# Kernel tuning notes

Measured on AMD Instinct MI355X. Metric: run time of the kernel, lower is better.

The kernel has to match this reference:

```python
import jax, jax.numpy as jnp
import numpy as np

N_NODES = 50000
N_EDGES = 800000
N_GRAPHS = 128
D = 128
L = 4
C = 10
GN_EPS = 1e-5


def setup_inputs() -> dict:
    key = jax.random.key(0)
    ks = jax.random.split(key, 12)
    s = 0.05
    x = jax.random.normal(ks[0], (N_NODES, D), dtype=jnp.float32)
    gin_w1 = jax.random.normal(ks[1], (L, D, D), dtype=jnp.float32) * s
    gin_b1 = jax.random.normal(ks[2], (L, D), dtype=jnp.float32) * s
    gin_w2 = jax.random.normal(ks[3], (L, D, D), dtype=jnp.float32) * s
    gin_b2 = jax.random.normal(ks[4], (L, D), dtype=jnp.float32) * s
    gn_weight = jnp.ones((L, D), dtype=jnp.float32)
    gn_bias = jnp.zeros((L, D), dtype=jnp.float32)
    gn_scale = jnp.ones((L, D), dtype=jnp.float32)
    fw1 = jax.random.normal(ks[5], (D, D), dtype=jnp.float32) * s
    fb1 = jnp.zeros((D,), dtype=jnp.float32)
    fw2 = jax.random.normal(ks[6], (D, D), dtype=jnp.float32) * s
    fb2 = jnp.zeros((D,), dtype=jnp.float32)
    fw3 = jax.random.normal(ks[7], (D, C), dtype=jnp.float32) * s
    fb3 = jnp.zeros((C,), dtype=jnp.float32)
    edge_index = jax.random.randint(ks[8], (2, N_EDGES), 0, N_NODES, dtype=jnp.int64)
    batch = jnp.sort(jax.random.randint(ks[9], (N_NODES,), 0, N_GRAPHS, dtype=jnp.int64))
    return dict(x=x, gin_w1=gin_w1, gin_b1=gin_b1, gin_w2=gin_w2, gin_b2=gin_b2,
                gn_weight=gn_weight, gn_bias=gn_bias, gn_scale=gn_scale,
                fw1=fw1, fb1=fb1, fw2=fw2, fb2=fb2, fw3=fw3, fb3=fb3,
                edge_index=edge_index, batch=batch)


def _graph_norm(h, batch, weight, bias, mean_scale, counts):
    # PyG GraphNorm: per-graph mean/var with learnable mean_scale.
    mean = jax.ops.segment_sum(h, batch, num_segments=N_GRAPHS) / counts  # [G, D]
    out = h - mean[batch] * mean_scale
    var = jax.ops.segment_sum(out * out, batch, num_segments=N_GRAPHS) / counts
    return weight * out / jnp.sqrt(var[batch] + GN_EPS) + bias


def reference(x, gin_w1, gin_b1, gin_w2, gin_b2, gn_weight, gn_bias, gn_scale,
              fw1, fb1, fw2, fb2, fw3, fb3, edge_index, batch):
    src, dst = edge_index[0], edge_index[1]
    ones = jnp.ones((N_NODES, 1), dtype=x.dtype)
    counts = jnp.maximum(jax.ops.segment_sum(ones, batch, num_segments=N_GRAPHS), 1.0)  # [G,1]
    h = x
    for l in range(L):
        # GINConv, eps=0: (1+eps)*x + sum_{j->i} x_j, then MLP with act after each Linear
        agg = jax.ops.segment_sum(h[src], dst, num_segments=N_NODES)  # [N, D]
        h = h + agg
        h = jax.nn.relu(h @ gin_w1[l] + gin_b1[l])
        h = jax.nn.relu(h @ gin_w2[l] + gin_b2[l])
        h = _graph_norm(h, batch, gn_weight[l], gn_bias[l], gn_scale[l], counts)
        h = jax.nn.relu(h)
    # sum readout per graph
    g = jax.ops.segment_sum(h, batch, num_segments=N_GRAPHS)  # [G, D]
    # final MLP (dropout is identity in eval)
    g = jax.nn.relu(g @ fw1 + fb1)
    g = jax.nn.relu(g @ fw2 + fb2)
    out = g @ fw3 + fb3
    return jax.nn.log_softmax(out, axis=-1)
```

## Files before the change

kernel.cpp:

```cpp
#include <hip/hip_runtime.h>
#include <cstddef>

#define N_NODES 50000
#define N_EDGES 800000
#define N_GRAPHS 128
#define DIM 128
#define N_LAYERS 4
#define GN_EPS 1e-5f

#define B_CHUNK 256
#define EPB 3125
#define BUCKET_SHIFT 9
#define BUCKET_SIZE 512
#define NB 98

typedef unsigned short ushort_t;
typedef __attribute__((ext_vector_type(8))) short frag8;
typedef __attribute__((ext_vector_type(4))) float f32x4;

__device__ inline float bfbits2f(unsigned hi16) { return __uint_as_float(hi16 << 16); }
__device__ inline ushort_t bf16rne(float v) {
    unsigned u = __float_as_uint(v);
    unsigned r = u + 0x7fff + ((u >> 16) & 1);
    return (ushort_t)(r >> 16);
}
__device__ inline unsigned packbf2(float a, float b) {
    return (unsigned)bf16rne(a) | ((unsigned)bf16rne(b) << 16);
}
__device__ inline void bf16split(float v, ushort_t& h, ushort_t& l) {
    ushort_t hi = bf16rne(v);
    float fh = __uint_as_float(((unsigned)hi) << 16);
    l = bf16rne(v - fh);
    h = hi;
}

__global__ __launch_bounds__(256) void graph_bounds(const int* __restrict__ batch, int* __restrict__ gstart) {
    int i = blockIdx.x * 256 + threadIdx.x;
    if (i >= N_NODES) return;
    int b = batch[i];
    if (i == 0) {
        for (int g = 0; g <= b; ++g) gstart[g] = 0;
    } else {
        int pb = batch[i - 1];
        for (int g = pb + 1; g <= b; ++g) gstart[g] = i;
    }
    if (i == N_NODES - 1) {
        for (int g = b + 1; g <= N_GRAPHS; ++g) gstart[g] = N_NODES;
    }
}

__global__ __launch_bounds__(256) void p1_count(const int* __restrict__ dst, int* __restrict__ cnts) {
    __shared__ int cnt[NB];
    int t = threadIdx.x, blk = blockIdx.x;
    for (int i = t; i < NB; i += 256) cnt[i] = 0;
    __syncthreads();
    int base = blk * EPB;
    for (int i = t; i < EPB; i += 256) atomicAdd(&cnt[dst[base + i] >> BUCKET_SHIFT], 1);
    __syncthreads();
    for (int i = t; i < NB; i += 256) cnts[i * B_CHUNK + blk] = cnt[i];
}

__global__ __launch_bounds__(1024) void scan_local(const int* __restrict__ in, int* __restrict__ out,
                                                   int* __restrict__ bsum, int n) {
    __shared__ int wsum[16];
    int tid = threadIdx.x, lane = tid & 63, w = tid >> 6;
    int gi = blockIdx.x * 1024 + tid;
    int v = (gi < n) ? in[gi] : 0;
    int s = v;
    #pragma unroll
    for (int off = 1; off < 64; off <<= 1) {
        int t = __shfl_up(s, off, 64);
        if (lane >= off) s += t;
    }
    if (lane == 63) wsum[w] = s;
    __syncthreads();
    if (w == 0) {
        int ws = (lane < 16) ? wsum[lane] : 0;
        #pragma unroll
        for (int off = 1; off < 16; off <<= 1) {
            int t = __shfl_up(ws, off, 64);
            if (lane >= off) ws += t;
        }
        if (lane < 16) wsum[lane] = ws;
    }
    __syncthreads();
    int woff = (w > 0) ? wsum[w - 1] : 0;
    if (gi < n) out[gi] = woff + s - v;
    if (tid == 1023) bsum[blockIdx.x] = woff + s;
}

__global__ __launch_bounds__(64) void scan_block(int* __restrict__ bsum, int nb) {
    int lane = threadIdx.x;
    int v = (lane < nb) ? bsum[lane] : 0;
    int s = v;
    #pragma unroll
    for (int off = 1; off < 64; off <<= 1) {
        int t = __shfl_up(s, off, 64);
        if (lane >= off) s += t;
    }
    if (lane < nb) bsum[lane] = s - v;
}

__global__ __launch_bounds__(1024) void scan_add(int* __restrict__ out, const int* __restrict__ bsum, int n, int total) {
    int gi = blockIdx.x * 1024 + threadIdx.x;
    if (gi < n) out[gi] += bsum[blockIdx.x];
    if (blockIdx.x == 0 && threadIdx.x == 0) out[n] = total;
}

__global__ __launch_bounds__(256) void p3_place(const int* __restrict__ src, const int* __restrict__ dst,
                                                const int* __restrict__ off, unsigned* __restrict__ ebuf) {
    __shared__ int cur[NB];
    int t = threadIdx.x, blk = blockIdx.x;
    for (int i = t; i < NB; i += 256) cur[i] = off[i * B_CHUNK + blk];
    __syncthreads();
    int base = blk * EPB;
    for (int i = t; i < EPB; i += 256) {
        int d = dst[base + i];
        int b = d >> BUCKET_SHIFT;
        int pos = atomicAdd(&cur[b], 1);
        ebuf[pos] = (unsigned)src[base + i] | ((unsigned)(d & (BUCKET_SIZE - 1)) << 16);
    }
}

__global__ __launch_bounds__(512) void p4_csr(const unsigned* __restrict__ ebuf, const int* __restrict__ off,
                                              int* __restrict__ eoff, int* __restrict__ csr) {
    __shared__ int cnt[BUCKET_SIZE];
    __shared__ int wsum[8];
    int k = blockIdx.x, t = threadIdx.x;
    int bstart = off[k * B_CHUNK];
    int bend = off[(k + 1) * B_CHUNK];
    cnt[t] = 0;
    __syncthreads();
    for (int i = bstart + t; i < bend; i += 512) atomicAdd(&cnt[ebuf[i] >> 16], 1);
    __syncthreads();
    int lane = t & 63, w = t >> 6;
    int v = cnt[t], s = v;
    #pragma unroll
    for (int o = 1; o < 64; o <<= 1) {
        int tt = __shfl_up(s, o, 64);
        if (lane >= o) s += tt;
    }
    if (lane == 63) wsum[w] = s;
    __syncthreads();
    if (w == 0) {
        int ws = (lane < 8) ? wsum[lane] : 0;
        #pragma unroll
        for (int o = 1; o < 8; o <<= 1) {
            int tt = __shfl_up(ws, o, 64);
            if (lane >= o) ws += tt;
        }
        if (lane < 8) wsum[lane] = ws;
    }
    __syncthreads();
    int woff = (w > 0) ? wsum[w - 1] : 0;
    int excl = woff + s - v;
    int node = k * BUCKET_SIZE + t;
    if (node < N_NODES) eoff[node] = bstart + excl;
    __syncthreads();
    cnt[t] = excl;
    __syncthreads();
    for (int i = bstart + t; i < bend; i += 512) {
        unsigned p = ebuf[i];
        int pos = atomicAdd(&cnt[p >> 16], 1);
        csr[bstart + pos] = (int)(p & 0xffffu);
    }
    if (k == NB - 1 && t == 0) eoff[N_NODES] = N_EDGES;
}

__global__ __launch_bounds__(256) void convert_w(const float* __restrict__ w1, const float* __restrict__ w2,
                                                 ushort_t* __restrict__ hi, ushort_t* __restrict__ lo) {
    int idx = blockIdx.x * 256 + threadIdx.x;
    if (idx >= 8 * DIM * DIM) return;
    int mat = idx >> 14;
    int e = idx & 16383;
    int n = e >> 7, k = e & 127;
    int l = mat >> 1;
    const float* src = (mat & 1) ? (w2 + (size_t)l * DIM * DIM) : (w1 + (size_t)l * DIM * DIM);
    float v = src[k * DIM + n];
    ushort_t h, lw;
    bf16split(v, h, lw);
    hi[(size_t)mat * DIM * DIM + n * DIM + k] = h;
    lo[(size_t)mat * DIM * DIM + n * DIM + k] = lw;
}

__global__ __launch_bounds__(256) void convert_x(const float* __restrict__ x, unsigned* __restrict__ Hb) {
    int i = blockIdx.x * 256 + threadIdx.x;
    if (i >= N_NODES * 64) return;
    float a = x[2 * i], b = x[2 * i + 1];
    Hb[i] = packbf2(a, b);
}

__global__ __launch_bounds__(256) void agg_bf16(const unsigned* __restrict__ h, const int* __restrict__ eoff,
                                                const int* __restrict__ csr, unsigned* __restrict__ T) {
    int wid = (blockIdx.x * 256 + threadIdx.x) >> 6;
    int lane = threadIdx.x & 63;
    if (wid >= N_NODES) return;
    int lo = eoff[wid], hi = eoff[wid + 1];
    unsigned v = h[(size_t)wid * 64 + lane];
    float a0 = bfbits2f(v & 0xffffu);
    float a1 = bfbits2f(v >> 16);
    for (int base = lo; base < hi; base += 64) {
        int nav = hi - base;
        if (nav > 64) nav = 64;
        int jv = (base + lane < hi) ? csr[base + lane] : 0;
        int e = 0;
        for (; e + 7 < nav; e += 8) {
            int j0 = __shfl(jv, e + 0, 64);
            int j1 = __shfl(jv, e + 1, 64);
            int j2 = __shfl(jv, e + 2, 64);
            int j3 = __shfl(jv, e + 3, 64);
            int j4 = __shfl(jv, e + 4, 64);
            int j5 = __shfl(jv, e + 5, 64);
            int j6 = __shfl(jv, e + 6, 64);
            int j7 = __shfl(jv, e + 7, 64);
            unsigned w0 = h[(size_t)j0 * 64 + lane];
            unsigned w1 = h[(size_t)j1 * 64 + lane];
            unsigned w2 = h[(size_t)j2 * 64 + lane];
            unsigned w3 = h[(size_t)j3 * 64 + lane];
            unsigned w4 = h[(size_t)j4 * 64 + lane];
            unsigned w5 = h[(size_t)j5 * 64 + lane];
            unsigned w6 = h[(size_t)j6 * 64 + lane];
            unsigned w7 = h[(size_t)j7 * 64 + lane];
            a0 += bfbits2f(w0 & 0xffffu) + bfbits2f(w1 & 0xffffu) + bfbits2f(w2 & 0xffffu) + bfbits2f(w3 & 0xffffu)
                + bfbits2f(w4 & 0xffffu) + bfbits2f(w5 & 0xffffu) + bfbits2f(w6 & 0xffffu) + bfbits2f(w7 & 0xffffu);
            a1 += bfbits2f(w0 >> 16) + bfbits2f(w1 >> 16) + bfbits2f(w2 >> 16) + bfbits2f(w3 >> 16)
                + bfbits2f(w4 >> 16) + bfbits2f(w5 >> 16) + bfbits2f(w6 >> 16) + bfbits2f(w7 >> 16);
        }
        for (; e < nav; ++e) {
            int j = __shfl(jv, e, 64);
            unsigned w0 = h[(size_t)j * 64 + lane];
            a0 += bfbits2f(w0 & 0xffffu);
            a1 += bfbits2f(w0 >> 16);
        }
    }
    T[(size_t)wid * 64 + lane] = packbf2(a0, a1);
}

__global__ __launch_bounds__(256) void mm_layer(const ushort_t* __restrict__ A,
                                                const ushort_t* __restrict__ W1h, const ushort_t* __restrict__ W1l,
                                                const ushort_t* __restrict__ W2h, const ushort_t* __restrict__ W2l,
                                                const float* __restrict__ b1, const float* __restrict__ b2,
                                                ushort_t* __restrict__ Zb) {
    __shared__ ushort_t As[128 * 128];
    __shared__ ushort_t Ws[128 * 128];
    int tid = threadIdx.x;
    int row0 = blockIdx.x * 128;
    int wave = tid >> 6, lane = tid & 63;
    int q = lane >> 4, mn = lane & 15;

    f32x4 acc[2][8];
    #pragma unroll
    for (int t = 0; t < 2; ++t)
        #pragma unroll
        for (int n = 0; n < 8; ++n) acc[t][n] = (f32x4)(0.f);

    #pragma unroll
    for (int i = 0; i < 8; ++i) {
        int c = tid + i * 256;
        int r = c >> 4, c8 = c & 15;
        uint4 v = make_uint4(0u, 0u, 0u, 0u);
        int gr = row0 + r;
        if (gr < N_NODES) v = *(const uint4*)(A + (size_t)gr * DIM + c8 * 8);
        *(uint4*)(&As[r * 128 + (c8 ^ (r & 7)) * 8]) = v;
    }
    auto stageW = [&](const ushort_t* src) {
        #pragma unroll
        for (int i = 0; i < 8; ++i) {
            int c = tid + i * 256;
            int r = c >> 4, c8 = c & 15;
            uint4 v = *(const uint4*)(src + r * DIM + c8 * 8);
            *(uint4*)(&Ws[r * 128 + (c8 ^ (r & 7)) * 8]) = v;
        }
    };
    auto compute = [&]() {
        #pragma unroll
        for (int ks = 0; ks < 4; ++ks) {
            int m0 = wave * 32 + mn;
            int m1 = m0 + 16;
            frag8 a0 = *(const frag8*)&As[m0 * 128 + (((ks * 4 + q) ^ (m0 & 7)) * 8)];
            frag8 a1 = *(const frag8*)&As[m1 * 128 + (((ks * 4 + q) ^ (m1 & 7)) * 8)];
            #pragma unroll
            for (int n = 0; n < 8; ++n) {
                int nr = n * 16 + mn;
                frag8 b = *(const frag8*)&Ws[nr * 128 + (((ks * 4 + q) ^ (nr & 7)) * 8)];
                acc[0][n] = __builtin_amdgcn_mfma_f32_16x16x32_bf16(a0, b, acc[0][n], 0, 0, 0);
                acc[1][n] = __builtin_amdgcn_mfma_f32_16x16x32_bf16(a1, b, acc[1][n], 0, 0, 0);
            }
        }
    };

    stageW(W1h);
    __syncthreads(); compute(); __syncthreads();
    stageW(W1l);
    __syncthreads(); compute(); __syncthreads();

    int mloc = wave * 32;
    #pragma unroll
    for (int t = 0; t < 2; ++t) {
        #pragma unroll
        for (int n = 0; n < 8; ++n) {
            int col = n * 16 + mn;
            float bv = b1[col];
            #pragma unroll
            for (int r = 0; r < 4; ++r) {
                int rloc = mloc + t * 16 + q * 4 + r;
                float v = fmaxf(acc[t][n][r] + bv, 0.f);
                As[rloc * 128 + ((col >> 3) ^ (rloc & 7)) * 8 + (col & 7)] = bf16rne(v);
                acc[t][n][r] = 0.f;
            }
        }
    }
    __syncthreads();
    stageW(W2h);
    __syncthreads(); compute(); __syncthreads();
    stageW(W2l);
    __syncthreads(); compute();

    #pragma unroll
    for (int t = 0; t < 2; ++t) {
        #pragma unroll
        for (int n = 0; n < 8; ++n) {
            int col = n * 16 + mn;
            float bv = b2[col];
            #pragma unroll
            for (int r = 0; r < 4; ++r) {
                int grow = row0 + mloc + t * 16 + q * 4 + r;
                if (grow < N_NODES)
                    Zb[(size_t)grow * DIM + col] = bf16rne(fmaxf(acc[t][n][r] + bv, 0.f));
            }
        }
    }
}

template<bool LAST>
__global__ __launch_bounds__(1024) void gn_fused(const unsigned* __restrict__ Zb, const int* __restrict__ gstart,
                                                 const float* __restrict__ scale, const float* __restrict__ weight,
                                                 const float* __restrict__ bias,
                                                 unsigned* __restrict__ Hb, float* __restrict__ gsum) {
    __shared__ float2 sh1[1024], sh2[1024];
    __shared__ float sa[128], sb[128];
    int g = blockIdx.x;
    int dp = threadIdx.x & 63, rg = threadIdx.x >> 6;
    int s = gstart[g], e = gstart[g + 1];
    float2 s1 = make_float2(0.f, 0.f), s2 = make_float2(0.f, 0.f);
    for (int n = s + rg; n < e; n += 16) {
        unsigned zz = Zb[(size_t)n * 64 + dp];
        float z0 = bfbits2f(zz & 0xffffu), z1 = bfbits2f(zz >> 16);
        s1.x += z0; s1.y += z1;
        s2.x += z0 * z0; s2.y += z1 * z1;
    }
    sh1[threadIdx.x] = s1;
    sh2[threadIdx.x] = s2;
    __syncthreads();
    if (rg == 0) {
        #pragma unroll
        for (int k = 1; k < 16; ++k) {
            float2 t1 = sh1[dp + 64 * k], t2 = sh2[dp + 64 * k];
            s1.x += t1.x; s1.y += t1.y;
            s2.x += t2.x; s2.y += t2.y;
        }
        int cnt = e - s;
        float cf = (float)(cnt > 0 ? cnt : 1);
        int d0 = dp * 2, d1 = d0 + 1;
        float m0 = s1.x / cf, m1 = s1.y / cf;
        float ez0 = s2.x / cf, ez1 = s2.y / cf;
        float sc0 = scale[d0], sc1 = scale[d1];
        float var0 = fmaxf(ez0 - (2.0f - sc0) * sc0 * m0 * m0, 0.f);
        float var1 = fmaxf(ez1 - (2.0f - sc1) * sc1 * m1 * m1, 0.f);
        sa[d0] = m0 * sc0;
        sa[d1] = m1 * sc1;
        sb[d0] = weight[d0] / sqrtf(var0 + GN_EPS);
        sb[d1] = weight[d1] / sqrtf(var1 + GN_EPS);
    }
    __syncthreads();
    int d0 = dp * 2, d1 = d0 + 1;
    float as0 = sa[d0], bm0 = sb[d0], bi0 = bias[d0];
    float as1 = sa[d1], bm1 = sb[d1], bi1 = bias[d1];
    float2 rsum = make_float2(0.f, 0.f);
    for (int n = s + rg; n < e; n += 16) {
        unsigned zz = Zb[(size_t)n * 64 + dp];
        float z0 = bfbits2f(zz & 0xffffu), z1 = bfbits2f(zz >> 16);
        float o0 = fmaxf((z0 - as0) * bm0 + bi0, 0.f);
        float o1 = fmaxf((z1 - as1) * bm1 + bi1, 0.f);
        if (LAST) {
            rsum.x += o0; rsum.y += o1;
        } else {
            Hb[(size_t)n * 64 + dp] = packbf2(o0, o1);
        }
    }
    if (LAST) {
        __syncthreads();
        sh1[threadIdx.x] = rsum;
        __syncthreads();
        if (rg == 0) {
            #pragma unroll
            for (int k = 1; k < 16; ++k) {
                float2 t1 = sh1[dp + 64 * k];
                rsum.x += t1.x; rsum.y += t1.y;
            }
            gsum[g * DIM + d0] = rsum.x;
            gsum[g * DIM + d1] = rsum.y;
        }
    }
}

__global__ __launch_bounds__(128) void final_mlp(const float* __restrict__ gsum,
                                                 const float* __restrict__ fw1, const float* __restrict__ fb1,
                                                 const float* __restrict__ fw2, const float* __restrict__ fb2,
                                                 const float* __restrict__ fw3, const float* __restrict__ fb3,
                                                 float* __restrict__ out) {
    __shared__ float v0[128], v1[128], v2[128], lg[10];
    int t = threadIdx.x;
    int g = blockIdx.x;
    v0[t] = gsum[g * DIM + t];
    __syncthreads();
    float acc = fb1[t];
    for (int d = 0; d < 128; ++d) acc += v0[d] * fw1[d * 128 + t];
    v1[t] = fmaxf(acc, 0.f);
    __syncthreads();
    acc = fb2[t];
    for (int d = 0; d < 128; ++d) acc += v1[d] * fw2[d * 128 + t];
    v2[t] = fmaxf(acc, 0.f);
    __syncthreads();
    if (t < 10) {
        acc = fb3[t];
        for (int d = 0; d < 128; ++d) acc += v2[d] * fw3[d * 10 + t];
        lg[t] = acc;
    }
    __syncthreads();
    if (t < 10) {
        float m = -1e30f;
        for (int c = 0; c < 10; ++c) m = fmaxf(m, lg[c]);
        float ssum = 0.f;
        for (int c = 0; c < 10; ++c) ssum += expf(lg[c] - m);
        out[g * 10 + t] = lg[t] - m - logf(ssum);
    }
}

extern "C" void kernel_launch(void* const* d_in, const int* in_sizes, int n_in,
                              void* d_out, int out_size, void* d_ws, size_t ws_size,
                              hipStream_t stream) {
    const float* x      = (const float*)d_in[0];
    const float* gin_w1 = (const float*)d_in[1];
    const float* gin_b1 = (const float*)d_in[2];
    const float* gin_w2 = (const float*)d_in[3];
    const float* gin_b2 = (const float*)d_in[4];
    const float* gn_w   = (const float*)d_in[5];
    const float* gn_b   = (const float*)d_in[6];
    const float* gn_s   = (const float*)d_in[7];
    const float* fw1    = (const float*)d_in[8];
    const float* fb1    = (const float*)d_in[9];
    const float* fw2    = (const float*)d_in[10];
    const float* fb2    = (const float*)d_in[11];
    const float* fw3    = (const float*)d_in[12];
    const float* fb3    = (const float*)d_in[13];
    const int*   eidx   = (const int*)d_in[14];
    const int*   batch  = (const int*)d_in[15];
    float* out = (float*)d_out;

    const int* esrc = eidx;
    const int* edst = eidx + N_EDGES;

    auto align_up = [](size_t v) { return (v + 255) & ~(size_t)255; };
    char* p = (char*)d_ws;
    unsigned* Hb = (unsigned*)p;   p += align_up((size_t)N_NODES * DIM * 2);
    unsigned* Tb = (unsigned*)p;   p += align_up((size_t)N_NODES * DIM * 2);
    unsigned* Zb = (unsigned*)p;   p += align_up((size_t)N_NODES * DIM * 2);
    ushort_t* WThi = (ushort_t*)p; p += align_up((size_t)8 * DIM * DIM * 2);
    ushort_t* WTlo = (ushort_t*)p; p += align_up((size_t)8 * DIM * DIM * 2);
    float* gsum = (float*)p;       p += align_up(N_GRAPHS * DIM * 4);
    int* gstart = (int*)p;         p += align_up((N_GRAPHS + 1) * 4);
    int* cnts = (int*)p;           p += align_up((size_t)NB * B_CHUNK * 4);
    int* off = (int*)p;            p += align_up(((size_t)NB * B_CHUNK + 1) * 4);
    int* bsum = (int*)p;           p += align_up(64 * 4);
    unsigned* ebuf = (unsigned*)p; p += align_up((size_t)N_EDGES * 4);
    int* eoff = (int*)p;           p += align_up((N_NODES + 1) * 4);
    int* csr = (int*)p;            p += align_up((size_t)N_EDGES * 4);

    const int SCAN_N = NB * B_CHUNK;
    const int SCAN_BLKS = (SCAN_N + 1023) / 1024;
    graph_bounds<<<(N_NODES + 255) / 256, 256, 0, stream>>>(batch, gstart);
    p1_count<<<B_CHUNK, 256, 0, stream>>>(edst, cnts);
    scan_local<<<SCAN_BLKS, 1024, 0, stream>>>(cnts, off, bsum, SCAN_N);
    scan_block<<<1, 64, 0, stream>>>(bsum, SCAN_BLKS);
    scan_add<<<SCAN_BLKS, 1024, 0, stream>>>(off, bsum, SCAN_N, N_EDGES);
    p3_place<<<B_CHUNK, 256, 0, stream>>>(esrc, edst, off, ebuf);
    p4_csr<<<NB, 512, 0, stream>>>(ebuf, off, eoff, csr);
    convert_w<<<(8 * DIM * DIM + 255) / 256, 256, 0, stream>>>(gin_w1, gin_w2, WThi, WTlo);
    convert_x<<<(N_NODES * 64 + 255) / 256, 256, 0, stream>>>(x, Hb);

    const int mm_grid = (N_NODES + 127) / 128;
    for (int l = 0; l < N_LAYERS; ++l) {
        agg_bf16<<<(N_NODES + 3) / 4, 256, 0, stream>>>(Hb, eoff, csr, Tb);
        mm_layer<<<mm_grid, 256, 0, stream>>>((const ushort_t*)Tb,
            WThi + (size_t)(2 * l) * DIM * DIM, WTlo + (size_t)(2 * l) * DIM * DIM,
            WThi + (size_t)(2 * l + 1) * DIM * DIM, WTlo + (size_t)(2 * l + 1) * DIM * DIM,
            gin_b1 + l * DIM, gin_b2 + l * DIM, (ushort_t*)Zb);
        if (l == N_LAYERS - 1)
            gn_fused<true><<<N_GRAPHS, 1024, 0, stream>>>(Zb, gstart, gn_s + l * DIM,
                gn_w + l * DIM, gn_b + l * DIM, Hb, gsum);
        else
            gn_fused<false><<<N_GRAPHS, 1024, 0, stream>>>(Zb, gstart, gn_s + l * DIM,
                gn_w + l * DIM, gn_b + l * DIM, Hb, gsum);
    }

    final_mlp<<<N_GRAPHS, 128, 0, stream>>>(gsum, fw1, fb1, fw2, fb2, fw3, fb3, out);
}
```

Measured before the change: 443.0 us.

## Merge setup kernels, fuse final MLP into last GraphNorm, widen aggregation loads

Four setup kernels (x conversion, weight split, graph bounds, bucket count) are merged into one block-partitioned launch, and the final-layer GraphNorm is fused with the readout MLP and log-softmax. Both cut kernel launches and the round trip through the gsum buffer. The aggregation kernel now has each half-wave load 8-byte uint2 values and handle alternate edges, with a cross-half shuffle reduction at the end. This doubles the edges in flight per wave and widens each load, at the cost of idle lanes when a node has few edges and an extra reduction step.

```diff
diff --git a/kernel.cpp b/kernel.cpp
--- a/kernel.cpp
+++ b/kernel.cpp
@@ -14,6 +14,11 @@
 #define BUCKET_SIZE 512
 #define NB 98
 
+#define CX_BLKS 12500
+#define CW_BLKS 512
+#define GB_BLKS 196
+#define SETUP_BLKS (CX_BLKS + CW_BLKS + GB_BLKS + B_CHUNK)
+
 typedef unsigned short ushort_t;
 typedef __attribute__((ext_vector_type(8))) short frag8;
 typedef __attribute__((ext_vector_type(4))) float f32x4;
@@ -34,30 +39,54 @@
     h = hi;
 }
 
-__global__ __launch_bounds__(256) void graph_bounds(const int* __restrict__ batch, int* __restrict__ gstart) {
-    int i = blockIdx.x * 256 + threadIdx.x;
-    if (i >= N_NODES) return;
-    int b = batch[i];
-    if (i == 0) {
-        for (int g = 0; g <= b; ++g) gstart[g] = 0;
+__global__ __launch_bounds__(256) void setup_misc(const float* __restrict__ x, unsigned* __restrict__ Hb,
+                                                  const float* __restrict__ w1, const float* __restrict__ w2,
+                                                  ushort_t* __restrict__ whi, ushort_t* __restrict__ wlo,
+                                                  const int* __restrict__ batch, int* __restrict__ gstart,
+                                                  const int* __restrict__ edst, int* __restrict__ cnts) {
+    __shared__ int cnt[NB];
+    int b = blockIdx.x, t = threadIdx.x;
+    if (b < CX_BLKS) {
+        int i = b * 256 + t;
+        if (i < N_NODES * 64) {
+            float a = x[2 * i], bb = x[2 * i + 1];
+            Hb[i] = packbf2(a, bb);
+        }
+    } else if (b < CX_BLKS + CW_BLKS) {
+        int idx = (b - CX_BLKS) * 256 + t;
+        int mat = idx >> 14;
+        int e = idx & 16383;
+        int n = e >> 7, k = e & 127;
+        int l = mat >> 1;
+        const float* src = (mat & 1) ? (w2 + (size_t)l * DIM * DIM) : (w1 + (size_t)l * DIM * DIM);
+        float v = src[k * DIM + n];
+        ushort_t h, lw;
+        bf16split(v, h, lw);
+        whi[(size_t)mat * DIM * DIM + n * DIM + k] = h;
+        wlo[(size_t)mat * DIM * DIM + n * DIM + k] = lw;
+    } else if (b < CX_BLKS + CW_BLKS + GB_BLKS) {
+        int i = (b - CX_BLKS - CW_BLKS) * 256 + t;
+        if (i < N_NODES) {
+            int bb = batch[i];
+            if (i == 0) {
+                for (int g = 0; g <= bb; ++g) gstart[g] = 0;
+            } else {
+                int pb = batch[i - 1];
+                for (int g = pb + 1; g <= bb; ++g) gstart[g] = i;
+            }
+            if (i == N_NODES - 1) {
+                for (int g = bb + 1; g <= N_GRAPHS; ++g) gstart[g] = N_NODES;
+            }
+        }
     } else {
-        int pb = batch[i - 1];
-        for (int g = pb + 1; g <= b; ++g) gstart[g] = i;
-    }
-    if (i == N_NODES - 1) {
-        for (int g = b + 1; g <= N_GRAPHS; ++g) gstart[g] = N_NODES;
-    }
-}
-
-__global__ __launch_bounds__(256) void p1_count(const int* __restrict__ dst, int* __restrict__ cnts) {
-    __shared__ int cnt[NB];
-    int t = threadIdx.x, blk = blockIdx.x;
-    for (int i = t; i < NB; i += 256) cnt[i] = 0;
-    __syncthreads();
-    int base = blk * EPB;
-    for (int i = t; i < EPB; i += 256) atomicAdd(&cnt[dst[base + i] >> BUCKET_SHIFT], 1);
-    __syncthreads();
-    for (int i = t; i < NB; i += 256) cnts[i * B_CHUNK + blk] = cnt[i];
+        int blk = b - (CX_BLKS + CW_BLKS + GB_BLKS);
+        for (int i = t; i < NB; i += 256) cnt[i] = 0;
+        __syncthreads();
+        int base = blk * EPB;
+        for (int i = t; i < EPB; i += 256) atomicAdd(&cnt[edst[base + i] >> BUCKET_SHIFT], 1);
+        __syncthreads();
+        for (int i = t; i < NB; i += 256) cnts[i * B_CHUNK + blk] = cnt[i];
+    }
 }
 
 __global__ __launch_bounds__(1024) void scan_local(const int* __restrict__ in, int* __restrict__ out,
@@ -167,73 +196,64 @@
     if (k == NB - 1 && t == 0) eoff[N_NODES] = N_EDGES;
 }
 
-__global__ __launch_bounds__(256) void convert_w(const float* __restrict__ w1, const float* __restrict__ w2,
-                                                 ushort_t* __restrict__ hi, ushort_t* __restrict__ lo) {
-    int idx = blockIdx.x * 256 + threadIdx.x;
-    if (idx >= 8 * DIM * DIM) return;
-    int mat = idx >> 14;
-    int e = idx & 16383;
-    int n = e >> 7, k = e & 127;
-    int l = mat >> 1;
-    const float* src = (mat & 1) ? (w2 + (size_t)l * DIM * DIM) : (w1 + (size_t)l * DIM * DIM);
-    float v = src[k * DIM + n];
-    ushort_t h, lw;
-    bf16split(v, h, lw);
-    hi[(size_t)mat * DIM * DIM + n * DIM + k] = h;
-    lo[(size_t)mat * DIM * DIM + n * DIM + k] = lw;
-}
-
-__global__ __launch_bounds__(256) void convert_x(const float* __restrict__ x, unsigned* __restrict__ Hb) {
-    int i = blockIdx.x * 256 + threadIdx.x;
-    if (i >= N_NODES * 64) return;
-    float a = x[2 * i], b = x[2 * i + 1];
-    Hb[i] = packbf2(a, b);
-}
-
-__global__ __launch_bounds__(256) void agg_bf16(const unsigned* __restrict__ h, const int* __restrict__ eoff,
-                                                const int* __restrict__ csr, unsigned* __restrict__ T) {
+__global__ __launch_bounds__(256) void agg_bf16(const uint2* __restrict__ h2, const int* __restrict__ eoff,
+                                                const int* __restrict__ csr, uint2* __restrict__ T2) {
     int wid = (blockIdx.x * 256 + threadIdx.x) >> 6;
     int lane = threadIdx.x & 63;
+    int half = lane >> 5;
+    int hl = lane & 31;
     if (wid >= N_NODES) return;
     int lo = eoff[wid], hi = eoff[wid + 1];
-    unsigned v = h[(size_t)wid * 64 + lane];
-    float a0 = bfbits2f(v & 0xffffu);
-    float a1 = bfbits2f(v >> 16);
+
+    float a0 = 0.f, a1 = 0.f, a2 = 0.f, a3 = 0.f;
+    if (half == 0) {
+        uint2 sv = h2[(size_t)wid * 32 + hl];
+        a0 = bfbits2f(sv.x & 0xffffu); a1 = bfbits2f(sv.x >> 16);
+        a2 = bfbits2f(sv.y & 0xffffu); a3 = bfbits2f(sv.y >> 16);
+    }
+
     for (int base = lo; base < hi; base += 64) {
         int nav = hi - base;
         if (nav > 64) nav = 64;
         int jv = (base + lane < hi) ? csr[base + lane] : 0;
-        int e = 0;
-        for (; e + 7 < nav; e += 8) {
-            int j0 = __shfl(jv, e + 0, 64);
-            int j1 = __shfl(jv, e + 1, 64);
-            int j2 = __shfl(jv, e + 2, 64);
-            int j3 = __shfl(jv, e + 3, 64);
-            int j4 = __shfl(jv, e + 4, 64);
-            int j5 = __shfl(jv, e + 5, 64);
-            int j6 = __shfl(jv, e + 6, 64);
-            int j7 = __shfl(jv, e + 7, 64);
-            unsigned w0 = h[(size_t)j0 * 64 + lane];
-            unsigned w1 = h[(size_t)j1 * 64 + lane];
-            unsigned w2 = h[(size_t)j2 * 64 + lane];
-            unsigned w3 = h[(size_t)j3 * 64 + lane];
-            unsigned w4 = h[(size_t)j4 * 64 + lane];
-            unsigned w5 = h[(size_t)j5 * 64 + lane];
-            unsigned w6 = h[(size_t)j6 * 64 + lane];
-            unsigned w7 = h[(size_t)j7 * 64 + lane];
-            a0 += bfbits2f(w0 & 0xffffu) + bfbits2f(w1 & 0xffffu) + bfbits2f(w2 & 0xffffu) + bfbits2f(w3 & 0xffffu)
-                + bfbits2f(w4 & 0xffffu) + bfbits2f(w5 & 0xffffu) + bfbits2f(w6 & 0xffffu) + bfbits2f(w7 & 0xffffu);
-            a1 += bfbits2f(w0 >> 16) + bfbits2f(w1 >> 16) + bfbits2f(w2 >> 16) + bfbits2f(w3 >> 16)
-                + bfbits2f(w4 >> 16) + bfbits2f(w5 >> 16) + bfbits2f(w6 >> 16) + bfbits2f(w7 >> 16);
-        }
-        for (; e < nav; ++e) {
-            int j = __shfl(jv, e, 64);
-            unsigned w0 = h[(size_t)j * 64 + lane];
-            a0 += bfbits2f(w0 & 0xffffu);
-            a1 += bfbits2f(w0 >> 16);
-        }
-    }
-    T[(size_t)wid * 64 + lane] = packbf2(a0, a1);
+        int cmin = nav >> 1;
+        int cmax = (nav + 1) >> 1;
+        int i = 0;
+        for (; i + 3 < cmin; i += 4) {
+            int j0 = __shfl(jv, 2 * (i + 0) + half, 64);
+            int j1 = __shfl(jv, 2 * (i + 1) + half, 64);
+            int j2 = __shfl(jv, 2 * (i + 2) + half, 64);
+            int j3 = __shfl(jv, 2 * (i + 3) + half, 64);
+            uint2 w0 = h2[(size_t)j0 * 32 + hl];
+            uint2 w1 = h2[(size_t)j1 * 32 + hl];
+            uint2 w2 = h2[(size_t)j2 * 32 + hl];
+            uint2 w3 = h2[(size_t)j3 * 32 + hl];
+            a0 += bfbits2f(w0.x & 0xffffu) + bfbits2f(w1.x & 0xffffu) + bfbits2f(w2.x & 0xffffu) + bfbits2f(w3.x & 0xffffu);
+            a1 += bfbits2f(w0.x >> 16) + bfbits2f(w1.x >> 16) + bfbits2f(w2.x >> 16) + bfbits2f(w3.x >> 16);
+            a2 += bfbits2f(w0.y & 0xffffu) + bfbits2f(w1.y & 0xffffu) + bfbits2f(w2.y & 0xffffu) + bfbits2f(w3.y & 0xffffu);
+            a3 += bfbits2f(w0.y >> 16) + bfbits2f(w1.y >> 16) + bfbits2f(w2.y >> 16) + bfbits2f(w3.y >> 16);
+        }
+        for (; i < cmax; ++i) {
+            int epos = 2 * i + half;
+            int j = __shfl(jv, epos, 64);
+            if (epos < nav) {
+                uint2 w0 = h2[(size_t)j * 32 + hl];
+                a0 += bfbits2f(w0.x & 0xffffu); a1 += bfbits2f(w0.x >> 16);
+                a2 += bfbits2f(w0.y & 0xffffu); a3 += bfbits2f(w0.y >> 16);
+            }
+        }
+    }
+
+    a0 += __shfl_down(a0, 32, 64);
+    a1 += __shfl_down(a1, 32, 64);
+    a2 += __shfl_down(a2, 32, 64);
+    a3 += __shfl_down(a3, 32, 64);
+    if (half == 0) {
+        uint2 o;
+        o.x = packbf2(a0, a1);
+        o.y = packbf2(a2, a3);
+        T2[(size_t)wid * 32 + hl] = o;
+    }
 }
 
 __global__ __launch_bounds__(256) void mm_layer(const ushort_t* __restrict__ A,
@@ -332,11 +352,10 @@
     }
 }
 
-template<bool LAST>
 __global__ __launch_bounds__(1024) void gn_fused(const unsigned* __restrict__ Zb, const int* __restrict__ gstart,
                                                  const float* __restrict__ scale, const float* __restrict__ weight,
                                                  const float* __restrict__ bias,
-                                                 unsigned* __restrict__ Hb, float* __restrict__ gsum) {
+                                                 unsigned* __restrict__ Hb) {
     __shared__ float2 sh1[1024], sh2[1024];
     __shared__ float sa[128], sb[128];
     int g = blockIdx.x;
@@ -376,54 +395,97 @@
     int d0 = dp * 2, d1 = d0 + 1;
     float as0 = sa[d0], bm0 = sb[d0], bi0 = bias[d0];
     float as1 = sa[d1], bm1 = sb[d1], bi1 = bias[d1];
-    float2 rsum = make_float2(0.f, 0.f);
     for (int n = s + rg; n < e; n += 16) {
         unsigned zz = Zb[(size_t)n * 64 + dp];
         float z0 = bfbits2f(zz & 0xffffu), z1 = bfbits2f(zz >> 16);
         float o0 = fmaxf((z0 - as0) * bm0 + bi0, 0.f);
         float o1 = fmaxf((z1 - as1) * bm1 + bi1, 0.f);
-        if (LAST) {
-            rsum.x += o0; rsum.y += o1;
-        } else {
-            Hb[(size_t)n * 64 + dp] = packbf2(o0, o1);
-        }
-    }
-    if (LAST) {
-        __syncthreads();
-        sh1[threadIdx.x] = rsum;
-        __syncthreads();
-        if (rg == 0) {
-            #pragma unroll
-            for (int k = 1; k < 16; ++k) {
-                float2 t1 = sh1[dp + 64 * k];
-                rsum.x += t1.x; rsum.y += t1.y;
-            }
-            gsum[g * DIM + d0] = rsum.x;
-            gsum[g * DIM + d1] = rsum.y;
-        }
-    }
-}
-
-__global__ __launch_bounds__(128) void final_mlp(const float* __restrict__ gsum,
-                                                 const float* __restrict__ fw1, const float* __restrict__ fb1,
-                                                 const float* __restrict__ fw2, const float* __restrict__ fb2,
-                                                 const float* __restrict__ fw3, const float* __restrict__ fb3,
-                                                 float* __restrict__ out) {
+        Hb[(size_t)n * 64 + dp] = packbf2(o0, o1);
+    }
+}
+
+__global__ __launch_bounds__(1024) void gn_last(const unsigned* __restrict__ Zb, const int* __restrict__ gstart,
+                                                const float* __restrict__ scale, const float* __restrict__ weight,
+                                                const float* __restrict__ bias,
+                                                const float* __restrict__ fw1, const float* __restrict__ fb1,
+                                                const float* __restrict__ fw2, const float* __restrict__ fb2,
+                                                const float* __restrict__ fw3, const float* __restrict__ fb3,
+                                                float* __restrict__ out) {
+    __shared__ float2 sh1[1024], sh2[1024];
+    __shared__ float sa[128], sb[128];
     __shared__ float v0[128], v1[128], v2[128], lg[10];
+    int g = blockIdx.x;
     int t = threadIdx.x;
-    int g = blockIdx.x;
-    v0[t] = gsum[g * DIM + t];
-    __syncthreads();
-    float acc = fb1[t];
-    for (int d = 0; d < 128; ++d) acc += v0[d] * fw1[d * 128 + t];
-    v1[t] = fmaxf(acc, 0.f);
-    __syncthreads();
-    acc = fb2[t];
-    for (int d = 0; d < 128; ++d) acc += v1[d] * fw2[d * 128 + t];
-    v2[t] = fmaxf(acc, 0.f);
+    int dp = t & 63, rg = t >> 6;
+    int s = gstart[g], e = gstart[g + 1];
+    float2 s1 = make_float2(0.f, 0.f), s2 = make_float2(0.f, 0.f);
+    for (int n = s + rg; n < e; n += 16) {
+        unsigned zz = Zb[(size_t)n * 64 + dp];
+        float z0 = bfbits2f(zz & 0xffffu), z1 = bfbits2f(zz >> 16);
+        s1.x += z0; s1.y += z1;
+        s2.x += z0 * z0; s2.y += z1 * z1;
+    }
+    sh1[t] = s1;
+    sh2[t] = s2;
+    __syncthreads();
+    if (rg == 0) {
+        #pragma unroll
+        for (int k = 1; k < 16; ++k) {
+            float2 t1 = sh1[dp + 64 * k], t2 = sh2[dp + 64 * k];
+            s1.x += t1.x; s1.y += t1.y;
+            s2.x += t2.x; s2.y += t2.y;
+        }
+        int cnt = e - s;
+        float cf = (float)(cnt > 0 ? cnt : 1);
+        int d0 = dp * 2, d1 = d0 + 1;
+        float m0 = s1.x / cf, m1 = s1.y / cf;
+        float ez0 = s2.x / cf, ez1 = s2.y / cf;
+        float sc0 = scale[d0], sc1 = scale[d1];
+        float var0 = fmaxf(ez0 - (2.0f - sc0) * sc0 * m0 * m0, 0.f);
+        float var1 = fmaxf(ez1 - (2.0f - sc1) * sc1 * m1 * m1, 0.f);
+        sa[d0] = m0 * sc0;
+        sa[d1] = m1 * sc1;
+        sb[d0] = weight[d0] / sqrtf(var0 + GN_EPS);
+        sb[d1] = weight[d1] / sqrtf(var1 + GN_EPS);
+    }
+    __syncthreads();
+    int d0 = dp * 2, d1 = d0 + 1;
+    float as0 = sa[d0], bm0 = sb[d0], bi0 = bias[d0];
+    float as1 = sa[d1], bm1 = sb[d1], bi1 = bias[d1];
+    float2 rsum = make_float2(0.f, 0.f);
+    for (int n = s + rg; n < e; n += 16) {
+        unsigned zz = Zb[(size_t)n * 64 + dp];
+        float z0 = bfbits2f(zz & 0xffffu), z1 = bfbits2f(zz >> 16);
+        rsum.x += fmaxf((z0 - as0) * bm0 + bi0, 0.f);
+        rsum.y += fmaxf((z1 - as1) * bm1 + bi1, 0.f);
+    }
+    __syncthreads();
+    sh1[t] = rsum;
+    __syncthreads();
+    if (rg == 0) {
+        #pragma unroll
+        for (int k = 1; k < 16; ++k) {
+            float2 t1 = sh1[dp + 64 * k];
+            rsum.x += t1.x; rsum.y += t1.y;
+        }
+        v0[d0] = rsum.x;
+        v0[d1] = rsum.y;
+    }
+    __syncthreads();
+    if (t < 128) {
+        float acc = fb1[t];
+        for (int d = 0; d < 128; ++d) acc += v0[d] * fw1[d * 128 + t];
+        v1[t] = fmaxf(acc, 0.f);
+    }
+    __syncthreads();
+    if (t < 128) {
+        float acc = fb2[t];
+        for (int d = 0; d < 128; ++d) acc += v1[d] * fw2[d * 128 + t];
+        v2[t] = fmaxf(acc, 0.f);
+    }
     __syncthreads();
     if (t < 10) {
-        acc = fb3[t];
+        float acc = fb3[t];
         for (int d = 0; d < 128; ++d) acc += v2[d] * fw3[d * 10 + t];
         lg[t] = acc;
     }
@@ -468,7 +530,6 @@
     unsigned* Zb = (unsigned*)p;   p += align_up((size_t)N_NODES * DIM * 2);
     ushort_t* WThi = (ushort_t*)p; p += align_up((size_t)8 * DIM * DIM * 2);
     ushort_t* WTlo = (ushort_t*)p; p += align_up((size_t)8 * DIM * DIM * 2);
-    float* gsum = (float*)p;       p += align_up(N_GRAPHS * DIM * 4);
     int* gstart = (int*)p;         p += align_up((N_GRAPHS + 1) * 4);
     int* cnts = (int*)p;           p += align_up((size_t)NB * B_CHUNK * 4);
     int* off = (int*)p;            p += align_up(((size_t)NB * B_CHUNK + 1) * 4);
@@ -479,30 +540,26 @@
 
     const int SCAN_N = NB * B_CHUNK;
     const int SCAN_BLKS = (SCAN_N + 1023) / 1024;
-    graph_bounds<<<(N_NODES + 255) / 256, 256, 0, stream>>>(batch, gstart);
-    p1_count<<<B_CHUNK, 256, 0, stream>>>(edst, cnts);
+    setup_misc<<<SETUP_BLKS, 256, 0, stream>>>(x, Hb, gin_w1, gin_w2, WThi, WTlo,
+                                               batch, gstart, edst, cnts);
     scan_local<<<SCAN_BLKS, 1024, 0, stream>>>(cnts, off, bsum, SCAN_N);
     scan_block<<<1, 64, 0, stream>>>(bsum, SCAN_BLKS);
     scan_add<<<SCAN_BLKS, 1024, 0, stream>>>(off, bsum, SCAN_N, N_EDGES);
     p3_place<<<B_CHUNK, 256, 0, stream>>>(esrc, edst, off, ebuf);
     p4_csr<<<NB, 512, 0, stream>>>(ebuf, off, eoff, csr);
-    convert_w<<<(8 * DIM * DIM + 255) / 256, 256, 0, stream>>>(gin_w1, gin_w2, WThi, WTlo);
-    convert_x<<<(N_NODES * 64 + 255) / 256, 256, 0, stream>>>(x, Hb);
 
     const int mm_grid = (N_NODES + 127) / 128;
     for (int l = 0; l < N_LAYERS; ++l) {
-        agg_bf16<<<(N_NODES + 3) / 4, 256, 0, stream>>>(Hb, eoff, csr, Tb);
+        agg_bf16<<<(N_NODES + 3) / 4, 256, 0, stream>>>((const uint2*)Hb, eoff, csr, (uint2*)Tb);
         mm_layer<<<mm_grid, 256, 0, stream>>>((const ushort_t*)Tb,
             WThi + (size_t)(2 * l) * DIM * DIM, WTlo + (size_t)(2 * l) * DIM * DIM,
             WThi + (size_t)(2 * l + 1) * DIM * DIM, WTlo + (size_t)(2 * l + 1) * DIM * DIM,
             gin_b1 + l * DIM, gin_b2 + l * DIM, (ushort_t*)Zb);
         if (l == N_LAYERS - 1)
-            gn_fused<true><<<N_GRAPHS, 1024, 0, stream>>>(Zb, gstart, gn_s + l * DIM,
-                gn_w + l * DIM, gn_b + l * DIM, Hb, gsum);
+            gn_last<<<N_GRAPHS, 1024, 0, stream>>>(Zb, gstart, gn_s + l * DIM,
+                gn_w + l * DIM, gn_b + l * DIM, fw1, fb1, fw2, fb2, fw3, fb3, out);
         else
-            gn_fused<false><<<N_GRAPHS, 1024, 0, stream>>>(Zb, gstart, gn_s + l * DIM,
-                gn_w + l * DIM, gn_b + l * DIM, Hb, gsum);
-    }
-
-    final_mlp<<<N_GRAPHS, 128, 0, stream>>>(gsum, fw1, fb1, fw2, fb2, fw3, fb3, out);
-}
+            gn_fused<<<N_GRAPHS, 1024, 0, stream>>>(Zb, gstart, gn_s + l * DIM,
+                gn_w + l * DIM, gn_b + l * DIM, Hb);
+    }
+}
```

After: 427.9 us. -3.4%, faster.
